# Kernel tuning notes

Measured on AMD Instinct MI355X. Metric: run time of the kernel, lower is better.

Reference implementation:

```python
import jax, jax.numpy as jnp
import numpy as np

NUM_HEADS = 16
SRC_FACTS = 4


def setup_inputs() -> dict:
    key = jax.random.key(0)
    k1, k2, k3, k4, k5 = jax.random.split(key, 5)
    B, S, H, Dh = 16, 512, NUM_HEADS, 64  # B = batch(4) * src_facts(4)
    D = H * Dh  # d_model = 1024
    pre_q = jax.random.normal(k1, (B, S, H, Dh), dtype=jnp.float32)
    pre_v = jax.random.normal(k2, (B, S, H, Dh), dtype=jnp.float32)
    pre_k = jax.random.normal(k3, (B, S, H, Dh), dtype=jnp.float32)
    attn_mask = jax.random.randint(k4, (B, S, S), 0, 2).astype(jnp.int32)
    output_weights = jax.random.normal(k5, (D, D), dtype=jnp.float32) / np.float32(np.sqrt(D))
    return {
        "pre_q": pre_q,
        "pre_v": pre_v,
        "pre_k": pre_k,
        "attn_mask": attn_mask,
        "output_weights": output_weights,
        "out_seq_len": 512,
        "d_model": 1024,
    }


def reference(pre_q, pre_v, pre_k, attn_mask, output_weights, out_seq_len, d_model):
    B, Sq, H, Dh = pre_q.shape
    # Original: K.sqrt(cast(d_model) // num_heads) -> sqrt(head_dim)
    scale = jnp.sqrt(jnp.float32(float(d_model) // H))
    mask = attn_mask.astype(jnp.float32)[:, None]  # (B, 1, q, k) broadcast over heads
    # scores: (B, H, q, k)
    scores = jnp.einsum("bqhd,bkhd->bhqk", pre_q, pre_k) / scale
    # multiplicative pre-mask + additive -1e9 on masked slots
    scores = scores * mask + (1.0 - mask) * jnp.float32(-1e9)
    # softmax then multiplicative post-mask
    attn = jax.nn.softmax(scores, axis=-1) * mask
    heads = jnp.einsum("bhqk,bkhd->bqhd", attn, pre_v)  # (B, q, H, Dh)
    out = heads.reshape(B, Sq, H * Dh) @ output_weights  # (B, q, d_model)
    return out.reshape(-1, SRC_FACTS, out_seq_len, d_model)
```

## Files before the change

### kernel.cpp

```cpp
#include <hip/hip_runtime.h>
#include <hip/hip_bf16.h>


typedef __bf16 bf16;
typedef bf16 bf16x8 __attribute__((ext_vector_type(8)));
typedef bf16 bf16x4 __attribute__((ext_vector_type(4)));
typedef float floatx4 __attribute__((ext_vector_type(4)));
typedef unsigned short ushort8 __attribute__((ext_vector_type(8)));
typedef unsigned long long u64;

#define MFMA32(A, B, C) __builtin_amdgcn_mfma_f32_16x16x32_bf16((A), (B), (C), 0, 0, 0)

namespace {
constexpr int S   = 512;
constexpr int H   = 16;
constexpr int Dh  = 64;
constexpr int D   = 1024;
constexpr int LDT = 72;
constexpr size_t QN = (size_t)16 * S * H * Dh;
constexpr size_t WN = (size_t)D * D;
}

__device__ __forceinline__ float fexp2(float x) {
#if defined(__HIP_DEVICE_COMPILE__) && __has_builtin(__builtin_amdgcn_exp2f)
    return __builtin_amdgcn_exp2f(x);
#else
    return exp2f(x);
#endif
}

__device__ __forceinline__ int sbfe1(unsigned bits, int bit) {
    return ((int)(bits << (31 - bit))) >> 31;
}

__global__ __launch_bounds__(256)
void prep_kernel(const float* __restrict__ Kf, const float* __restrict__ Vf,
                 const float* __restrict__ Wf, const int* __restrict__ Mg,
                 bf16* __restrict__ Kc, bf16* __restrict__ Vt,
                 bf16* __restrict__ Wt, u64* __restrict__ MB)
{
    __shared__ bf16 Ts[64 * LDT];
    const int blk = blockIdx.x, tid = threadIdx.x;

    if (blk < 4096) {
        const int i = blk * 256 + tid;
        const float* fs = Kf + (size_t)i * 8;
        bf16x8 v;
#pragma unroll
        for (int j = 0; j < 8; ++j) v[j] = (bf16)fs[j];
        *(bf16x8*)(Kc + (size_t)i * 8) = v;
    } else if (blk < 6144) {
        const int bk2 = blk - 4096;
        const int bh  = bk2 >> 3, st = bk2 & 7;
        const int b   = bh >> 4, h = bh & 15;
        const int r   = tid >> 2, c = (tid & 3) * 16;
        const float* src = Vf + ((size_t)((b * S + st * 64 + r) * H + h)) * Dh + c;
#pragma unroll
        for (int i = 0; i < 16; ++i)
            Ts[(c + i) * LDT + r] = (bf16)src[i];
        __syncthreads();
        bf16* dst = Vt + ((size_t)bh * 64 + r) * S + st * 64 + c;
        *(ushort8*)dst       = *(const ushort8*)&Ts[r * LDT + c];
        *(ushort8*)(dst + 8) = *(const ushort8*)&Ts[r * LDT + c + 8];
    } else if (blk < 6400) {
        const int bk2 = blk - 6144;
        const int nb  = bk2 & 15, kb = bk2 >> 4;
        const int r   = tid >> 2, c = (tid & 3) * 16;
        const float* src = Wf + (size_t)(kb * 64 + r) * D + nb * 64 + c;
#pragma unroll
        for (int i = 0; i < 16; ++i)
            Ts[(c + i) * LDT + r] = (bf16)src[i];
        __syncthreads();
        bf16* dst = Wt + (size_t)(nb * 64 + r) * D + kb * 64 + c;
        *(ushort8*)dst       = *(const ushort8*)&Ts[r * LDT + c];
        *(ushort8*)(dst + 8) = *(const ushort8*)&Ts[r * LDT + c + 8];
    } else {
        const int bk2  = blk - 6400;
        const int lane = tid & 63;
        const int idx4 = bk2 * 4 + (tid >> 6);
        const int row  = idx4 >> 1;
        const int half = idx4 & 1;
#pragma unroll
        for (int r = 0; r < 4; ++r) {
            int mv = Mg[(size_t)row * 512 + half * 256 + r * 64 + lane];
            u64 bm = __ballot(mv != 0);
            if (lane == 0) MB[(size_t)row * 8 + half * 4 + r] = bm;
        }
    }
}

__global__ __launch_bounds__(256, 4)
void attn_kernel(const float* __restrict__ Qg, const bf16* __restrict__ Kc,
                 const bf16* __restrict__ Vtg, const u64* __restrict__ MB,
                 bf16* __restrict__ heads)
{
    __shared__ bf16 Ks[64 * LDT];
    __shared__ bf16 Vt[64 * LDT];

    const int tid  = threadIdx.x;
    const int lane = tid & 63;
    const int wave = tid >> 6;
    const int l15  = lane & 15;
    const int quad = lane >> 4;

    const int blk = blockIdx.x;
    const int h   = blk & 15;
    const int qt  = (blk >> 4) & 7;
    const int b   = blk >> 7;
    const int qw  = qt * 64 + wave * 16;

    constexpr float QSCL = 0.125f * 1.44269504088896340736f;
    bf16x8 aq0, aq1;
    {
        const float* qb = Qg + ((size_t)((b * S + qw + l15) * H + h)) * Dh + quad * 8;
        floatx4 f0 = *(const floatx4*)qb;
        floatx4 f1 = *(const floatx4*)(qb + 4);
        floatx4 f2 = *(const floatx4*)(qb + 32);
        floatx4 f3 = *(const floatx4*)(qb + 36);
#pragma unroll
        for (int j = 0; j < 4; ++j) {
            aq0[j]     = (bf16)(f0[j] * QSCL);
            aq0[j + 4] = (bf16)(f1[j] * QSCL);
            aq1[j]     = (bf16)(f2[j] * QSCL);
            aq1[j + 4] = (bf16)(f3[j] * QSCL);
        }
    }

    float rsum = 0.f;
    floatx4 O[4];
#pragma unroll
    for (int i = 0; i < 4; ++i) O[i] = floatx4{0.f, 0.f, 0.f, 0.f};

    const u64* mbrow = MB + ((size_t)b * S + qw + l15) * 8;
    const bf16* vplane = Vtg + (size_t)(b * 16 + h) * 64 * S;

    const int sr = tid >> 2, sc_ = (tid & 3) * 16;
    const int kperm = ((sr >> 5) << 5) | (((sr & 15) >> 2) << 3)
                    | (((sr >> 4) & 1) << 2) | (sr & 3);

    for (int kt = 0; kt < 8; ++kt) {
        const int kb = kt * 64;
        const bf16* ksrc = Kc + ((size_t)((b * S + kb + kperm) * H + h)) * Dh + sc_;
        const bf16* vsrc = vplane + (size_t)sr * S + kb + sc_;
        ushort8 k0 = *(const ushort8*)ksrc;
        ushort8 k1 = *(const ushort8*)(ksrc + 8);
        ushort8 v0 = *(const ushort8*)vsrc;
        ushort8 v1 = *(const ushort8*)(vsrc + 8);
        u64 m64 = mbrow[kt];

        __syncthreads();
        *(ushort8*)&Ks[sr * LDT + sc_]     = k0;
        *(ushort8*)&Ks[sr * LDT + sc_ + 8] = k1;
        *(ushort8*)&Vt[sr * LDT + sc_]     = v0;
        *(ushort8*)&Vt[sr * LDT + sc_ + 8] = v1;
        __syncthreads();

        const unsigned qlo = (unsigned)(m64 >> (quad * 8));
        const unsigned qhi = (unsigned)(m64 >> (quad * 8 + 32));

        bf16x8 pB[2];
#pragma unroll
        for (int mt = 0; mt < 4; ++mt) {
            bf16x8 ak0 = *(const bf16x8*)&Ks[(mt * 16 + l15) * LDT + quad * 8];
            bf16x8 ak1 = *(const bf16x8*)&Ks[(mt * 16 + l15) * LDT + quad * 8 + 32];
            floatx4 acc = floatx4{0.f, 0.f, 0.f, 0.f};
            acc = MFMA32(ak0, aq0, acc);
            acc = MFMA32(ak1, aq1, acc);
            const int block = mt >> 1, tile = mt & 1;
            const unsigned bits = (block ? qhi : qlo) >> (tile * 4);
#pragma unroll
            for (int reg = 0; reg < 4; ++reg) {
                float e = fexp2(acc[reg]);
                int sx = sbfe1(bits, reg);
                float p = __uint_as_float(__float_as_uint(e) & (unsigned)sx);
                rsum += p;
                pB[block][tile * 4 + reg] = (bf16)p;
            }
        }

#pragma unroll
        for (int block = 0; block < 2; ++block) {
#pragma unroll
            for (int mt = 0; mt < 4; ++mt) {
                bf16x8 av = *(const bf16x8*)&Vt[(mt * 16 + l15) * LDT + block * 32 + quad * 8];
                O[mt] = MFMA32(av, pB[block], O[mt]);
            }
        }
    }

    rsum += __shfl_xor(rsum, 16, 64);
    rsum += __shfl_xor(rsum, 32, 64);
    const float inv = (rsum > 0.f) ? (1.f / rsum) : 0.f;

    bf16* hrow = heads + ((size_t)((b * S + qw + l15) * H + h)) * Dh;
#pragma unroll
    for (int mt = 0; mt < 4; ++mt) {
        bf16x4 h4;
#pragma unroll
        for (int reg = 0; reg < 4; ++reg) h4[reg] = (bf16)(O[mt][reg] * inv);
        *(bf16x4*)&hrow[mt * 16 + quad * 4] = h4;
    }
}

__global__ __launch_bounds__(256)
void proj_kernel(const bf16* __restrict__ A, const bf16* __restrict__ Wt,
                 float* __restrict__ out)
{
    __shared__ bf16 As[128 * LDT];
    __shared__ bf16 Ws[128 * LDT];

    const int tid  = threadIdx.x;
    const int lane = tid & 63;
    const int wave = tid >> 6;
    const int l15  = lane & 15;
    const int quad = lane >> 4;

    const int nb = blockIdx.x & 7;
    const int mb = blockIdx.x >> 3;
    const int mbase = mb * 128, nbase = nb * 128;
    const int wm = (wave & 1) * 64, wn = (wave >> 1) * 64;

    const int pr = tid >> 1, pc = (tid & 1) * 32;

    floatx4 O[4][4];
#pragma unroll
    for (int mt = 0; mt < 4; ++mt)
#pragma unroll
        for (int nt = 0; nt < 4; ++nt) O[mt][nt] = floatx4{0.f, 0.f, 0.f, 0.f};

    for (int kt = 0; kt < 16; ++kt) {
        const int kb = kt * 64;
        const bf16* asrc = A  + (size_t)(mbase + pr) * D + kb + pc;
        const bf16* wsrc = Wt + (size_t)(nbase + pr) * D + kb + pc;
        ushort8 a0 = *(const ushort8*)asrc;
        ushort8 a1 = *(const ushort8*)(asrc + 8);
        ushort8 a2 = *(const ushort8*)(asrc + 16);
        ushort8 a3 = *(const ushort8*)(asrc + 24);
        ushort8 w0 = *(const ushort8*)wsrc;
        ushort8 w1 = *(const ushort8*)(wsrc + 8);
        ushort8 w2 = *(const ushort8*)(wsrc + 16);
        ushort8 w3 = *(const ushort8*)(wsrc + 24);

        __syncthreads();
        *(ushort8*)&As[pr * LDT + pc]      = a0;
        *(ushort8*)&As[pr * LDT + pc + 8]  = a1;
        *(ushort8*)&As[pr * LDT + pc + 16] = a2;
        *(ushort8*)&As[pr * LDT + pc + 24] = a3;
        *(ushort8*)&Ws[pr * LDT + pc]      = w0;
        *(ushort8*)&Ws[pr * LDT + pc + 8]  = w1;
        *(ushort8*)&Ws[pr * LDT + pc + 16] = w2;
        *(ushort8*)&Ws[pr * LDT + pc + 24] = w3;
        __syncthreads();

        bf16x8 fa[4][2];
#pragma unroll
        for (int mt = 0; mt < 4; ++mt) {
            fa[mt][0] = *(const bf16x8*)&As[(wm + mt * 16 + l15) * LDT + quad * 8];
            fa[mt][1] = *(const bf16x8*)&As[(wm + mt * 16 + l15) * LDT + quad * 8 + 32];
        }
#pragma unroll
        for (int nt = 0; nt < 4; ++nt) {
            bf16x8 fb0 = *(const bf16x8*)&Ws[(wn + nt * 16 + l15) * LDT + quad * 8];
            bf16x8 fb1 = *(const bf16x8*)&Ws[(wn + nt * 16 + l15) * LDT + quad * 8 + 32];
#pragma unroll
            for (int mt = 0; mt < 4; ++mt) {
                O[mt][nt] = MFMA32(fa[mt][0], fb0, O[mt][nt]);
                O[mt][nt] = MFMA32(fa[mt][1], fb1, O[mt][nt]);
            }
        }
    }

#pragma unroll
    for (int mt = 0; mt < 4; ++mt) {
#pragma unroll
        for (int nt = 0; nt < 4; ++nt) {
#pragma unroll
            for (int reg = 0; reg < 4; ++reg) {
                const int m = mbase + wm + mt * 16 + quad * 4 + reg;
                const int n = nbase + wn + nt * 16 + l15;
                out[(size_t)m * D + n] = O[mt][nt][reg];
            }
        }
    }
}

extern "C" void kernel_launch(void* const* d_in, const int* in_sizes, int n_in,
                              void* d_out, int out_size, void* d_ws, size_t ws_size,
                              hipStream_t stream)
{
    const float* pre_q = (const float*)d_in[0];
    const float* pre_v = (const float*)d_in[1];
    const float* pre_k = (const float*)d_in[2];
    const int*   mask  = (const int*)d_in[3];
    const float* Wg    = (const float*)d_in[4];
    float* out = (float*)d_out;

    bf16* Kc    = (bf16*)d_ws;
    bf16* Vt    = Kc + QN;
    bf16* Wt    = Vt + QN;
    bf16* heads = Wt + WN;
    u64*  MB    = (u64*)(heads + QN);

    prep_kernel<<<10496, 256, 0, stream>>>(pre_k, pre_v, Wg, mask, Kc, Vt, Wt, MB);
    attn_kernel<<<2048, 256, 0, stream>>>(pre_q, Kc, Vt, MB, heads);
    proj_kernel<<<512, 256, 0, stream>>>(heads, Wt, out);
}
```

Measured before the change: 215.1 us.

## Switch attention kernel to 32x32x16 MFMA with 128-query tiles

Rewrites the attention kernel's inner loops to use the 32x32x16 bf16 MFMA instead of 16x16x32, with each wave owning 32 query rows and each block 128 queries. The grid is halved, so each staged K/V tile in shared memory serves twice as many queries, and the K permutation, mask bit extraction and output layout are remapped to match. This aims to cut shared-memory and global K/V traffic per query and to use the larger matrix instruction more efficiently. In exchange it raises per-thread accumulator registers and lowers the block count, which may hurt occupancy.

```diff
diff --git a/kernel.cpp b/kernel.cpp
--- a/kernel.cpp
+++ b/kernel.cpp
@@ -6,10 +6,12 @@
 typedef bf16 bf16x8 __attribute__((ext_vector_type(8)));
 typedef bf16 bf16x4 __attribute__((ext_vector_type(4)));
 typedef float floatx4 __attribute__((ext_vector_type(4)));
+typedef float floatx16 __attribute__((ext_vector_type(16)));
 typedef unsigned short ushort8 __attribute__((ext_vector_type(8)));
 typedef unsigned long long u64;
 
-#define MFMA32(A, B, C) __builtin_amdgcn_mfma_f32_16x16x32_bf16((A), (B), (C), 0, 0, 0)
+#define MFMA32(A, B, C)  __builtin_amdgcn_mfma_f32_16x16x32_bf16((A), (B), (C), 0, 0, 0)
+#define MFMA32x32(A, B, C) __builtin_amdgcn_mfma_f32_32x32x16_bf16((A), (B), (C), 0, 0, 0)
 
 namespace {
 constexpr int S   = 512;
@@ -100,43 +102,43 @@
     const int tid  = threadIdx.x;
     const int lane = tid & 63;
     const int wave = tid >> 6;
-    const int l15  = lane & 15;
-    const int quad = lane >> 4;
+    const int l31  = lane & 31;
+    const int half = lane >> 5;
 
     const int blk = blockIdx.x;
     const int h   = blk & 15;
-    const int qt  = (blk >> 4) & 7;
-    const int b   = blk >> 7;
-    const int qw  = qt * 64 + wave * 16;
+    const int qt  = (blk >> 4) & 3;
+    const int b   = blk >> 6;
+    const int qw  = qt * 128 + wave * 32;
 
     constexpr float QSCL = 0.125f * 1.44269504088896340736f;
-    bf16x8 aq0, aq1;
+    bf16x8 aq[4];
     {
-        const float* qb = Qg + ((size_t)((b * S + qw + l15) * H + h)) * Dh + quad * 8;
-        floatx4 f0 = *(const floatx4*)qb;
-        floatx4 f1 = *(const floatx4*)(qb + 4);
-        floatx4 f2 = *(const floatx4*)(qb + 32);
-        floatx4 f3 = *(const floatx4*)(qb + 36);
-#pragma unroll
-        for (int j = 0; j < 4; ++j) {
-            aq0[j]     = (bf16)(f0[j] * QSCL);
-            aq0[j + 4] = (bf16)(f1[j] * QSCL);
-            aq1[j]     = (bf16)(f2[j] * QSCL);
-            aq1[j + 4] = (bf16)(f3[j] * QSCL);
+        const float* qb = Qg + ((size_t)((b * S + qw + l31) * H + h)) * Dh + half * 8;
+#pragma unroll
+        for (int ds = 0; ds < 4; ++ds) {
+            floatx4 f0 = *(const floatx4*)(qb + ds * 16);
+            floatx4 f1 = *(const floatx4*)(qb + ds * 16 + 4);
+#pragma unroll
+            for (int j = 0; j < 4; ++j) {
+                aq[ds][j]     = (bf16)(f0[j] * QSCL);
+                aq[ds][j + 4] = (bf16)(f1[j] * QSCL);
+            }
         }
     }
 
     float rsum = 0.f;
-    floatx4 O[4];
-#pragma unroll
-    for (int i = 0; i < 4; ++i) O[i] = floatx4{0.f, 0.f, 0.f, 0.f};
-
-    const u64* mbrow = MB + ((size_t)b * S + qw + l15) * 8;
+    floatx16 O[2];
+#pragma unroll
+    for (int dt = 0; dt < 2; ++dt)
+#pragma unroll
+        for (int i = 0; i < 16; ++i) O[dt][i] = 0.f;
+
+    const u64* mbrow = MB + ((size_t)b * S + qw + l31) * 8;
     const bf16* vplane = Vtg + (size_t)(b * 16 + h) * 64 * S;
 
     const int sr = tid >> 2, sc_ = (tid & 3) * 16;
-    const int kperm = ((sr >> 5) << 5) | (((sr & 15) >> 2) << 3)
-                    | (((sr >> 4) & 1) << 2) | (sr & 3);
+    const int kperm = (sr & 0x33) | ((sr & 4) << 1) | ((sr & 8) >> 1);
 
     for (int kt = 0; kt < 8; ++kt) {
         const int kb = kt * 64;
@@ -155,50 +157,50 @@
         *(ushort8*)&Vt[sr * LDT + sc_ + 8] = v1;
         __syncthreads();
 
-        const unsigned qlo = (unsigned)(m64 >> (quad * 8));
-        const unsigned qhi = (unsigned)(m64 >> (quad * 8 + 32));
-
-        bf16x8 pB[2];
-#pragma unroll
-        for (int mt = 0; mt < 4; ++mt) {
-            bf16x8 ak0 = *(const bf16x8*)&Ks[(mt * 16 + l15) * LDT + quad * 8];
-            bf16x8 ak1 = *(const bf16x8*)&Ks[(mt * 16 + l15) * LDT + quad * 8 + 32];
-            floatx4 acc = floatx4{0.f, 0.f, 0.f, 0.f};
-            acc = MFMA32(ak0, aq0, acc);
-            acc = MFMA32(ak1, aq1, acc);
-            const int block = mt >> 1, tile = mt & 1;
-            const unsigned bits = (block ? qhi : qlo) >> (tile * 4);
-#pragma unroll
-            for (int reg = 0; reg < 4; ++reg) {
-                float e = fexp2(acc[reg]);
-                int sx = sbfe1(bits, reg);
+        bf16x8 pB[4];
+#pragma unroll
+        for (int t = 0; t < 2; ++t) {
+            floatx16 acc;
+#pragma unroll
+            for (int i = 0; i < 16; ++i) acc[i] = 0.f;
+#pragma unroll
+            for (int ds = 0; ds < 4; ++ds) {
+                bf16x8 ak = *(const bf16x8*)&Ks[(t * 32 + l31) * LDT + ds * 16 + half * 8];
+                acc = MFMA32x32(ak, aq[ds], acc);
+            }
+            const unsigned w = (unsigned)(m64 >> (t * 32 + half * 8));
+#pragma unroll
+            for (int r = 0; r < 16; ++r) {
+                float e = fexp2(acc[r]);
+                int sx = sbfe1(w, (r >> 3) * 16 + (r & 7));
                 float p = __uint_as_float(__float_as_uint(e) & (unsigned)sx);
                 rsum += p;
-                pB[block][tile * 4 + reg] = (bf16)p;
-            }
-        }
-
-#pragma unroll
-        for (int block = 0; block < 2; ++block) {
-#pragma unroll
-            for (int mt = 0; mt < 4; ++mt) {
-                bf16x8 av = *(const bf16x8*)&Vt[(mt * 16 + l15) * LDT + block * 32 + quad * 8];
-                O[mt] = MFMA32(av, pB[block], O[mt]);
-            }
-        }
-    }
-
-    rsum += __shfl_xor(rsum, 16, 64);
+                pB[t * 2 + (r >> 3)][r & 7] = (bf16)p;
+            }
+        }
+
+#pragma unroll
+        for (int dt = 0; dt < 2; ++dt)
+#pragma unroll
+            for (int s_ = 0; s_ < 4; ++s_) {
+                bf16x8 av = *(const bf16x8*)&Vt[(dt * 32 + l31) * LDT + s_ * 16 + half * 8];
+                O[dt] = MFMA32x32(av, pB[s_], O[dt]);
+            }
+    }
+
     rsum += __shfl_xor(rsum, 32, 64);
     const float inv = (rsum > 0.f) ? (1.f / rsum) : 0.f;
 
-    bf16* hrow = heads + ((size_t)((b * S + qw + l15) * H + h)) * Dh;
-#pragma unroll
-    for (int mt = 0; mt < 4; ++mt) {
-        bf16x4 h4;
-#pragma unroll
-        for (int reg = 0; reg < 4; ++reg) h4[reg] = (bf16)(O[mt][reg] * inv);
-        *(bf16x4*)&hrow[mt * 16 + quad * 4] = h4;
+    bf16* hrow = heads + ((size_t)((b * S + qw + l31) * H + h)) * Dh;
+#pragma unroll
+    for (int dt = 0; dt < 2; ++dt) {
+#pragma unroll
+        for (int g = 0; g < 4; ++g) {
+            bf16x4 h4;
+#pragma unroll
+            for (int j = 0; j < 4; ++j) h4[j] = (bf16)(O[dt][g * 4 + j] * inv);
+            *(bf16x4*)&hrow[dt * 32 + g * 8 + half * 4] = h4;
+        }
     }
 }
 
@@ -302,6 +304,6 @@
     u64*  MB    = (u64*)(heads + QN);
 
     prep_kernel<<<10496, 256, 0, stream>>>(pre_k, pre_v, Wg, mask, Kc, Vt, Wt, MB);
-    attn_kernel<<<2048, 256, 0, stream>>>(pre_q, Kc, Vt, MB, heads);
+    attn_kernel<<<1024, 256, 0, stream>>>(pre_q, Kc, Vt, MB, heads);
     proj_kernel<<<512, 256, 0, stream>>>(heads, Wt, out);
 }
```

After: 211.6 us. Within noise of the previous version (-1.6%).
